# Kernel optimization log

Hardware: AMD Instinct MI355X
Metric: run time of the kernel (lower is better)

The kernel has to match this reference:

```python
import jax, jax.numpy as jnp
import numpy as np

EPS = 1e-6

def setup_inputs() -> dict:
    key = jax.random.key(0)
    ks = jax.random.split(key, 8)
    S, B, I, D, L = 1024, 16, 1024, 1024, 2
    std = np.sqrt(2.0 / (5.0 * I))
    inp = {
        "input": jax.random.normal(ks[0], (S, B, I), jnp.float32),
        "h0": jnp.zeros((L, B, D), jnp.float32),
        "extra0": jnp.zeros((L, B, 3 * D), jnp.float32),
        "W0": jax.random.normal(ks[1], (4 * D, I), jnp.float32) * std,
        "b0": jnp.zeros((4 * D,), jnp.float32).at[2 * D:3 * D].set(
            jax.random.uniform(ks[2], (D,), jnp.float32, 3.0, 6.0)),
        "r0": jnp.zeros((4 * D,), jnp.float32),
        "W1": jax.random.normal(ks[3], (4 * D, D), jnp.float32) * std,
        "b1": jnp.zeros((4 * D,), jnp.float32).at[2 * D:3 * D].set(
            jax.random.uniform(ks[4], (D,), jnp.float32, 3.0, 6.0)),
        "r1": jnp.zeros((4 * D,), jnp.float32),
    }
    return inp

def _cell(x, c, n, h, m, W, b, r):
    # x: (B, in), states: (B, D), W: (4D, in), b/r: (4D,)
    D = h.shape[-1]
    pre = x @ W.T + b  # (B, 4D)
    rz, ri, rf, ro = jnp.split(r, 4)
    z_pre = pre[:, 0 * D:1 * D] + rz * h
    i_pre = pre[:, 1 * D:2 * D] + ri * h
    f_pre = pre[:, 2 * D:3 * D] + rf * h
    o_pre = pre[:, 3 * D:4 * D] + ro * h
    z_t = jnp.tanh(z_pre)
    o_t = jax.nn.sigmoid(o_pre)
    m_new = jnp.maximum(f_pre + m, i_pre)
    f_t = jnp.exp(f_pre + m - m_new)
    i_t = jnp.exp(i_pre - m_new)
    c_new = f_t * c + i_t * z_t
    n_new = f_t * n + i_t
    h_new = o_t * (c_new / (jnp.abs(n_new) + EPS))
    return h_new, c_new, n_new, m_new

def _run(input, h0, extra0, params):
    D = h0.shape[-1]
    c0 = extra0[:, :, 0 * D:1 * D]
    n0 = extra0[:, :, 1 * D:2 * D]
    m0 = extra0[:, :, 2 * D:3 * D]

    def step(carry, x_t):
        h, c, n, m = carry  # each (L, B, D)
        x = x_t
        hs, cs, ns, ms = [], [], [], []
        for l, (W, b, r) in enumerate(params):
            h_new, c_new, n_new, m_new = _cell(x, c[l], n[l], h[l], m[l], W, b, r)
            hs.append(h_new); cs.append(c_new); ns.append(n_new); ms.append(m_new)
            x = h_new
        carry = (jnp.stack(hs), jnp.stack(cs), jnp.stack(ns), jnp.stack(ms))
        return carry, x

    (h_f, c_f, n_f, m_f), output = jax.lax.scan(step, (h0, c0, n0, m0), input)
    extra_f = jnp.concatenate([c_f, n_f, m_f], axis=-1)
    return output, h_f, extra_f

def reference(input, h0, extra0, W0, b0, r0, W1, b1, r1):
    params = [(W0, b0, r0), (W1, b1, r1)]
    return _run(input, h0, extra0, params)
```

## Files before the change

### kernel.cpp

```cpp
#include <hip/hip_runtime.h>
#include <hip/hip_bf16.h>

#define S_LEN  1024
#define BATCH  16
#define IDIM   1024
#define DDIM   1024
#define NG     4096
#define BD     16384
#define LAYERS 2
#define PF     16
#define PFP    8
#define NSEG   8

typedef __attribute__((ext_vector_type(8))) short   short8;
typedef __attribute__((ext_vector_type(4))) float   floatx4;
typedef __attribute__((address_space(1))) void      as1_void;
typedef __attribute__((address_space(3))) void      as3_void;

#define L2E  1.4426950408889634f
#define LN2  0.6931471805599453f

#define EXP2F(x) exp2f(x)

static __device__ __forceinline__ unsigned short f2bf(float x) {
    unsigned int u = __float_as_uint(x);
    return (unsigned short)((u + 0x7fffu + ((u >> 16) & 1u)) >> 16);
}

__global__ void detect_dtype(const void* w, int* flag)
{
    const __hip_bfloat16* p = (const __hip_bfloat16*)w;
    float mx = 0.0f;
    for (int i = threadIdx.x; i < 4096; i += 64) {
        float v = __bfloat162float(p[i]);
        float a = fabsf(v);
        if (!(a == a)) a = 1e30f;
        mx = fmaxf(mx, a);
    }
#pragma unroll
    for (int o = 32; o > 0; o >>= 1)
        mx = fmaxf(mx, __shfl_down(mx, o, 64));
    if (threadIdx.x == 0) *flag = (mx > 1e3f) ? 1 : 0;
}

__global__ void to_bf16(const void* src, size_t elem_off, const int* flag,
                        unsigned short* dst, int n)
{
    const int i = blockIdx.x * 256 + threadIdx.x;
    if (i >= n) return;
    if (*flag) dst[i] = f2bf(((const float*)src)[elem_off + i]);
    else       dst[i] = ((const unsigned short*)src)[elem_off + i];
}

__global__ void prep_small(const void* __restrict__ h0,
                           const void* __restrict__ extra0,
                           const void* __restrict__ b0s, const void* __restrict__ r0s,
                           const void* __restrict__ b1s, const void* __restrict__ r1s,
                           const int* __restrict__ flag,
                           float* __restrict__ state,
                           float* __restrict__ pb,
                           int* __restrict__ rflag)
{
    const int blk = blockIdx.x;
    const int fl = *flag;

    if (blk < 128) {
        const int idx = blk * 256 + threadIdx.x;
        const int l  = idx / BD;
        const int bd = idx % BD;
        const int b = bd >> 10, d = bd & 1023;
        float* st = state + (size_t)l * 4 * BD;
        const size_t eoff = ((size_t)l * BATCH + b) * (3 * DDIM);
        float cv, nv, mv, hv;
        if (fl) {
            const float* e = (const float*)extra0 + eoff;
            cv = e[d]; nv = e[DDIM + d]; mv = e[2 * DDIM + d];
            hv = ((const float*)h0)[(size_t)l * BD + bd];
        } else {
            const __hip_bfloat16* e = (const __hip_bfloat16*)extra0 + eoff;
            cv = __bfloat162float(e[d]);
            nv = __bfloat162float(e[DDIM + d]);
            mv = __bfloat162float(e[2 * DDIM + d]);
            hv = __bfloat162float(((const __hip_bfloat16*)h0)[(size_t)l * BD + bd]);
        }
        st[0 * BD + bd] = cv;
        st[1 * BD + bd] = nv;
        st[2 * BD + bd] = mv * L2E;
        st[3 * BD + bd] = hv;
        return;
    }

    const int which = blk - 128;
    const void* src = (which == 0) ? b0s : (which == 1) ? r0s
                    : (which == 2) ? b1s : r1s;
    float* dst = pb + (size_t)which * NG;
    int nz = 0;
#pragma unroll
    for (int j = 0; j < NG / 256; j++) {
        const int i = j * 256 + threadIdx.x;
        float v;
        if (fl) {
            v = ((const float*)src)[i];
            nz |= (v != 0.0f);
        } else {
            const unsigned short u = ((const unsigned short*)src)[i];
            nz |= ((u & 0x7fffu) != 0);
            v = __bfloat162float(((const __hip_bfloat16*)src)[i]);
        }
        dst[i] = v;
    }
    if (which == 1 || which == 3) {
        __shared__ int s[4];
        const int w = threadIdx.x >> 6;
        const int any = __any(nz) ? 1 : 0;
        if ((threadIdx.x & 63) == 0) s[w] = any;
        __syncthreads();
        if (threadIdx.x == 0) rflag[which >> 1] = !(s[0] | s[1] | s[2] | s[3]);
    }
}

__global__ __launch_bounds__(256, 2)
void gemm_bias(const __hip_bfloat16* __restrict__ A,
               const __hip_bfloat16* __restrict__ W,
               const float* __restrict__ bias,
               unsigned short* __restrict__ out,
               const int* __restrict__ rflag)
{
    constexpr int K = 1024;
    __shared__ alignas(16) __hip_bfloat16 sA[128 * 32];
    __shared__ alignas(16) __hip_bfloat16 sB[128 * 32];

    const int t  = threadIdx.x;
    const int m0 = blockIdx.y * 128;
    const int nb = blockIdx.x;
    const int lr = t & 15;
    const int q  = (t >> 4) & 3;
    const int w  = t >> 6;
    const int wm = w >> 1, wn = w & 1;
    const int sr = t >> 2;
    const int sk = (t & 3) * 8;

    floatx4 acc[4][4] = {};

    const __hip_bfloat16* Ab = A + (size_t)(m0 + sr) * K + sk;
    const int wrow = ((sr >> 5) << 10) + nb * 32 + (sr & 31);
    const __hip_bfloat16* Wb = W + (size_t)wrow * K + sk;

    for (int k0 = 0; k0 < K; k0 += 32) {
        __syncthreads();
        __builtin_amdgcn_global_load_lds((as1_void*)(Ab + k0),            (as3_void*)&sA[sr * 32 + sk],        16, 0, 0);
        __builtin_amdgcn_global_load_lds((as1_void*)(Ab + 64 * K + k0),   (as3_void*)&sA[(sr + 64) * 32 + sk], 16, 0, 0);
        __builtin_amdgcn_global_load_lds((as1_void*)(Wb + k0),            (as3_void*)&sB[sr * 32 + sk],        16, 0, 0);
        __builtin_amdgcn_global_load_lds((as1_void*)(Wb + 2048 * K + k0), (as3_void*)&sB[(sr + 64) * 32 + sk], 16, 0, 0);
        __syncthreads();

        short8 af[4], bf[4];
#pragma unroll
        for (int i = 0; i < 4; i++)
            af[i] = *(const short8*)&sA[(wm * 64 + i * 16 + lr) * 32 + q * 8];
#pragma unroll
        for (int j = 0; j < 4; j++)
            bf[j] = *(const short8*)&sB[(j * 32 + wn * 16 + lr) * 32 + q * 8];
#pragma unroll
        for (int i = 0; i < 4; i++)
#pragma unroll
            for (int j = 0; j < 4; j++)
                acc[i][j] = __builtin_amdgcn_mfma_f32_16x16x32_bf16(af[i], bf[j], acc[i][j], 0, 0, 0);
    }

    const int d = nb * 32 + wn * 16 + lr;
    const float sc[4] = {2.0f * L2E, L2E, L2E, L2E};
    float bb[4];
#pragma unroll
    for (int g = 0; g < 4; g++) bb[g] = sc[g] * bias[g * 1024 + d];

    const int rfast = *rflag;

#pragma unroll
    for (int i = 0; i < 4; i++) {
#pragma unroll
        for (int reg = 0; reg < 4; reg++) {
            const int row = m0 + wm * 64 + i * 16 + q * 4 + reg;
            float v[4];
#pragma unroll
            for (int g = 0; g < 4; g++)
                v[g] = acc[i][g][reg] * sc[g] + bb[g];
            if (rfast) {
                const float zv = v[0];
                const float e2 = EXP2F(-fabsf(zv));
                v[0] = copysignf((1.0f - e2) * __builtin_amdgcn_rcpf(1.0f + e2), zv);
                v[3] = __builtin_amdgcn_rcpf(1.0f + EXP2F(-v[3]));
            }
            union { unsigned short us[4]; uint2 u2; } pk;
#pragma unroll
            for (int g = 0; g < 4; g++) pk.us[g] = f2bf(v[g]);
            *(uint2*)(out + (size_t)row * NG + d * 4) = pk.u2;
        }
    }
}

__global__ void scan_passA(const unsigned int* __restrict__ pre,
                           const int* __restrict__ rflag,
                           float* __restrict__ smry, int T)
{
    if (!*rflag) return;
    const int gid = blockIdx.x * 256 + threadIdx.x;
    const int chain = gid & (BD - 1);
    const int seg = gid >> 14;
    const int SEG = T >> 3;
    const int b = chain >> 10, d = chain & 1023;

    const size_t stp = 32768;
    const unsigned int* p = pre + (size_t)b * 2048 + (size_t)d * 2
                              + (size_t)(seg * SEG) * stp;

    float alpha = 0.0f, mu = -3e38f, Bh = 0.0f, Nh = 0.0f;

    unsigned int k0[PFP], k1[PFP];
#pragma unroll
    for (int u = 0; u < PFP; u++) {
        const uint2 v = *(const uint2*)(p + (size_t)u * stp);
        k0[u] = v.x; k1[u] = v.y;
    }

    for (int t = 0; t < SEG; t += PFP) {
#pragma unroll
        for (int u = 0; u < PFP; u++) {
            const float zt = __uint_as_float(k0[u] << 16);
            const float i2 = __uint_as_float(k0[u] & 0xffff0000u);
            const float f2 = __uint_as_float(k1[u] << 16);

            const uint2 nv = *(const uint2*)(p + (size_t)(t + u + PFP) * stp);
            k0[u] = nv.x; k1[u] = nv.y;

            alpha += f2;
            const float e  = i2 - alpha;
            const float mn = fmaxf(mu, e);
            const float s  = EXP2F(mu - mn);
            const float w  = EXP2F(e - mn);
            Bh = fmaf(Bh, s, w * zt);
            Nh = fmaf(Nh, s, w);
            mu = mn;
        }
    }

    smry[0 * NSEG * BD + seg * BD + chain] = alpha;
    smry[1 * NSEG * BD + seg * BD + chain] = alpha + mu;
    smry[2 * NSEG * BD + seg * BD + chain] = Bh;
    smry[3 * NSEG * BD + seg * BD + chain] = Nh;
}

__global__ void scan_mid(const float* __restrict__ smry,
                         const int* __restrict__ rflag,
                         const float* __restrict__ state,
                         float* __restrict__ seginit, int T)
{
    if (!*rflag) return;
    const int idx = blockIdx.x * 256 + threadIdx.x;
    float c  = state[0 * BD + idx];
    float n  = state[1 * BD + idx];
    float m2 = state[2 * BD + idx];
#pragma unroll
    for (int s = 0; s < NSEG; s++) {
        seginit[0 * NSEG * BD + s * BD + idx] = c;
        seginit[1 * NSEG * BD + s * BD + idx] = n;
        seginit[2 * NSEG * BD + s * BD + idx] = m2;
        const float A    = smry[0 * NSEG * BD + s * BD + idx];
        const float bmax = smry[1 * NSEG * BD + s * BD + idx];
        const float Bh   = smry[2 * NSEG * BD + s * BD + idx];
        const float Nh   = smry[3 * NSEG * BD + s * BD + idx];
        const float mn = fmaxf(m2 + A, bmax);
        const float sc = EXP2F(m2 + A - mn);
        const float w  = EXP2F(bmax - mn);
        c  = fmaf(sc, c, w * Bh);
        n  = fmaf(sc, n, w * Nh);
        m2 = mn;
    }
}

template<int MODE>
__global__ void scan_passB(const unsigned int* __restrict__ pre,
                           const float* __restrict__ seginit,
                           const int* __restrict__ rflag,
                           float* __restrict__ state,
                           unsigned short* __restrict__ hseq,
                           void* __restrict__ gout, size_t gout_eoff,
                           const int* __restrict__ flag, int T)
{
    if (!*rflag) return;
    const int gid = blockIdx.x * 256 + threadIdx.x;
    const int chain = gid & (BD - 1);
    const int seg = gid >> 14;
    const int SEG = T >> 3;
    const int t0s = seg * SEG;
    const int b = chain >> 10, d = chain & 1023;
    const int fl = *flag;

    float c  = seginit[0 * NSEG * BD + seg * BD + chain];
    float n  = seginit[1 * NSEG * BD + seg * BD + chain];
    float m2 = seginit[2 * NSEG * BD + seg * BD + chain];

    const size_t stp = 32768;
    const unsigned int* p = pre + (size_t)b * 2048 + (size_t)d * 2
                              + (size_t)t0s * stp;

    unsigned short* hb = hseq + (size_t)b * DDIM + d + (size_t)t0s * BD;
    float*          fo = (float*)gout + gout_eoff + (size_t)b * DDIM + d + (size_t)t0s * BD;
    unsigned short* bo = (unsigned short*)gout + gout_eoff + (size_t)b * DDIM + d + (size_t)t0s * BD;

    float h = 0.0f;
    unsigned int k0[PFP], k1[PFP];
#pragma unroll
    for (int u = 0; u < PFP; u++) {
        const uint2 v = *(const uint2*)(p + (size_t)u * stp);
        k0[u] = v.x; k1[u] = v.y;
    }

    for (int t = 0; t < SEG; t += PFP) {
#pragma unroll
        for (int u = 0; u < PFP; u++) {
            const float zt = __uint_as_float(k0[u] << 16);
            const float i2 = __uint_as_float(k0[u] & 0xffff0000u);
            const float f2 = __uint_as_float(k1[u] << 16);
            const float ot = __uint_as_float(k1[u] & 0xffff0000u);

            const uint2 nv = *(const uint2*)(p + (size_t)(t + u + PFP) * stp);
            k0[u] = nv.x; k1[u] = nv.y;

            const float fm = f2 + m2;
            const float mn = fmaxf(fm, i2);
            const float ft = EXP2F(fm - mn);
            const float it = EXP2F(i2 - mn);

            c  = fmaf(ft, c, it * zt);
            n  = fmaf(ft, n, it);
            m2 = mn;
            h  = ot * c * __builtin_amdgcn_rcpf(fabsf(n) + 1e-6f);

            const size_t toff = (size_t)(t + u) * BD;
            if (MODE == 0)      hb[toff] = f2bf(h);
            else if (fl)        fo[toff] = h;
            else                bo[toff] = f2bf(h);
        }
    }

    if (seg == NSEG - 1) {
        state[0 * BD + chain] = c;
        state[1 * BD + chain] = n;
        state[2 * BD + chain] = m2;
        state[3 * BD + chain] = h;
    }
}

template<int MODE>
__global__ void slstm_scan(const unsigned int* __restrict__ pre,
                           const float* __restrict__ r,
                           float* __restrict__ state,
                           unsigned short* __restrict__ hseq,
                           void* __restrict__ gout, size_t gout_eoff,
                           const int* __restrict__ flag,
                           const int* __restrict__ rflag, int T, int pgate)
{
    const int rfast = *rflag;
    if (pgate && rfast) return;

    const int idx = blockIdx.x * 64 + threadIdx.x;
    const int b = idx >> 10;
    const int d = idx & 1023;
    const int fl = *flag;

    const float rz = r[d]            * (2.0f * L2E);
    const float ri = r[DDIM + d]     * L2E;
    const float rf = r[2 * DDIM + d] * L2E;
    const float ro = r[3 * DDIM + d] * L2E;

    float c  = state[0 * BD + idx];
    float n  = state[1 * BD + idx];
    float m2 = state[2 * BD + idx];
    float h  = state[3 * BD + idx];

    const size_t stp = 32768;
    const unsigned int* p = pre + (size_t)b * 2048 + (size_t)d * 2;

    unsigned short* hb = hseq + (size_t)b * DDIM + d;
    float*          fo = (float*)gout + gout_eoff + (size_t)b * DDIM + d;
    unsigned short* bo = (unsigned short*)gout + gout_eoff + (size_t)b * DDIM + d;

    unsigned int k0[PF], k1[PF];
#pragma unroll
    for (int u = 0; u < PF; u++) {
        const uint2 v = *(const uint2*)(p + (size_t)u * stp);
        k0[u] = v.x; k1[u] = v.y;
    }

    if (rfast) {
        for (int t8 = 0; t8 < T; t8 += PF) {
#pragma unroll
            for (int u = 0; u < PF; u++) {
                const float zt = __uint_as_float(k0[u] << 16);
                const float i2 = __uint_as_float(k0[u] & 0xffff0000u);
                const float f2 = __uint_as_float(k1[u] << 16);
                const float ot = __uint_as_float(k1[u] & 0xffff0000u);

                const uint2 nv = *(const uint2*)(p + (size_t)(t8 + u + PF) * stp);
                k0[u] = nv.x; k1[u] = nv.y;

                const float fm = f2 + m2;
                const float mn = fmaxf(fm, i2);
                const float ft = EXP2F(fm - mn);
                const float it = EXP2F(i2 - mn);

                c  = fmaf(ft, c, it * zt);
                n  = fmaf(ft, n, it);
                m2 = mn;
                h  = ot * c * __builtin_amdgcn_rcpf(fabsf(n) + 1e-6f);

                const size_t toff = (size_t)(t8 + u) * BD;
                if (MODE == 0)      hb[toff] = f2bf(h);
                else if (fl)        fo[toff] = h;
                else                bo[toff] = f2bf(h);
            }
        }
    } else {
        for (int t8 = 0; t8 < T; t8 += PF) {
#pragma unroll
            for (int u = 0; u < PF; u++) {
                float z2 = __uint_as_float(k0[u] << 16);
                float i2 = __uint_as_float(k0[u] & 0xffff0000u);
                float f2 = __uint_as_float(k1[u] << 16);
                float o2 = __uint_as_float(k1[u] & 0xffff0000u);

                const uint2 nv = *(const uint2*)(p + (size_t)(t8 + u + PF) * stp);
                k0[u] = nv.x; k1[u] = nv.y;

                z2 = fmaf(rz, h, z2);
                i2 = fmaf(ri, h, i2);
                f2 = fmaf(rf, h, f2);
                o2 = fmaf(ro, h, o2);

                const float fm = f2 + m2;
                const float mn = fmaxf(fm, i2);
                const float ft = EXP2F(fm - mn);
                const float it = EXP2F(i2 - mn);

                const float e2 = EXP2F(-fabsf(z2));
                const float zt = copysignf((1.0f - e2) * __builtin_amdgcn_rcpf(1.0f + e2), z2);
                const float ot = __builtin_amdgcn_rcpf(1.0f + EXP2F(-o2));

                c  = ft * c + it * zt;
                n  = ft * n + it;
                m2 = mn;
                h  = ot * c * __builtin_amdgcn_rcpf(fabsf(n) + 1e-6f);

                const size_t toff = (size_t)(t8 + u) * BD;
                if (MODE == 0)      hb[toff] = f2bf(h);
                else if (fl)        fo[toff] = h;
                else                bo[toff] = f2bf(h);
            }
        }
    }

    state[0 * BD + idx] = c;
    state[1 * BD + idx] = n;
    state[2 * BD + idx] = m2;
    state[3 * BD + idx] = h;
}

__global__ void finalize(const float* __restrict__ state,
                         void* __restrict__ out,
                         const int* __restrict__ flag)
{
    const int idx = blockIdx.x * 256 + threadIdx.x;
    const int l  = idx / BD;
    const int bd = idx % BD;
    const int b = bd >> 10, d = bd & 1023;
    const float* st = state + (size_t)l * 4 * BD;
    const float cv = st[0 * BD + bd], nv = st[1 * BD + bd];
    const float mv = st[2 * BD + bd] * LN2;
    const float hv = st[3 * BD + bd];

    const size_t hoff = (size_t)S_LEN * BD + idx;
    const size_t eoff = (size_t)S_LEN * BD + (size_t)LAYERS * BD
                      + ((size_t)l * BATCH + b) * (3 * DDIM);
    if (*flag) {
        float* o = (float*)out;
        o[hoff] = hv;
        o[eoff + d] = cv; o[eoff + DDIM + d] = nv; o[eoff + 2 * DDIM + d] = mv;
    } else {
        unsigned short* o = (unsigned short*)out;
        o[hoff] = f2bf(hv);
        o[eoff + d]            = f2bf(cv);
        o[eoff + DDIM + d]     = f2bf(nv);
        o[eoff + 2 * DDIM + d] = f2bf(mv);
    }
}

__global__ void zero_out_k(void* __restrict__ out, const int* __restrict__ flag,
                           int out_size)
{
    const size_t i = (size_t)blockIdx.x * 256 + threadIdx.x;
    const size_t nb = (size_t)out_size * ((*flag) ? 4 : 2);
    char* o = (char*)out;
    for (size_t j = i * 4; j < (i + 1) * 4 && j < nb; j++) o[j] = 0;
}

extern "C" void kernel_launch(void* const* d_in, const int* in_sizes, int n_in,
                              void* d_out, int out_size, void* d_ws, size_t ws_size,
                              hipStream_t stream)
{
    const void* input  = d_in[0];
    const void* h0     = d_in[1];
    const void* extra0 = d_in[2];
    const void* W0     = d_in[3];
    const void* b0     = d_in[4];
    const void* r0     = d_in[5];
    const void* W1     = d_in[6];
    const void* b1     = d_in[7];
    const void* r1     = d_in[8];

    const size_t FLAG_B  = 256;
    const size_t STATE_B = (size_t)LAYERS * 4 * BD * 4;
    const size_t W_B     = (size_t)NG * IDIM * 2;
    const size_t PB_B    = (size_t)4 * NG * 4;
    const size_t SM_B    = (size_t)4 * NSEG * BD * 4;
    const size_t SI_B    = (size_t)3 * NSEG * BD * 4;
    const size_t FIXED   = FLAG_B + STATE_B + 2 * W_B + PB_B + SM_B + SI_B;

    int T = 0;
    for (int cand = S_LEN; cand >= 8; cand >>= 1) {
        size_t need = FIXED
                    + (size_t)cand * BD * 2
                    + (size_t)cand * BD * 2
                    + (size_t)(cand + PF) * BATCH * NG * 2;
        if (need <= ws_size) { T = cand; break; }
    }

    char* ws = (char*)d_ws;
    int*   flag  = (int*)ws;
    int*   rflag = flag + 1;
    float* state = (float*)(ws + FLAG_B);
    __hip_bfloat16* W0b = (__hip_bfloat16*)(ws + FLAG_B + STATE_B);
    __hip_bfloat16* W1b = W0b + (size_t)NG * IDIM;
    float* pb    = (float*)(ws + FLAG_B + STATE_B + 2 * W_B);
    float* b0f = pb, *r0f = pb + NG, *b1f = pb + 2 * NG, *r1f = pb + 3 * NG;
    float* smry    = (float*)(ws + FLAG_B + STATE_B + 2 * W_B + PB_B);
    float* seginit = smry + (size_t)4 * NSEG * BD;
    unsigned short* Ain  = (unsigned short*)(ws + FIXED);
    unsigned short* hseq = Ain + (size_t)T * BD;
    unsigned short* pre  = hseq + (size_t)T * BD;

    detect_dtype<<<dim3(1), dim3(64), 0, stream>>>(W0, flag);

    if (T == 0) {
        zero_out_k<<<dim3((out_size + 255) / 256), dim3(256), 0, stream>>>(d_out, flag, out_size);
        return;
    }

    const int WN = NG * IDIM;
    to_bf16<<<dim3(WN / 256), dim3(256), 0, stream>>>(W0, 0, flag, (unsigned short*)W0b, WN);
    to_bf16<<<dim3(WN / 256), dim3(256), 0, stream>>>(W1, 0, flag, (unsigned short*)W1b, WN);

    prep_small<<<dim3(132), dim3(256), 0, stream>>>(h0, extra0, b0, r0, b1, r1,
                                                    flag, state, pb, rflag);

    const dim3 gemmGrid(32, (T * BATCH) / 128);
    const dim3 scanGrid(BD / 64);
    const dim3 passGrid((BD * NSEG) / 256);
    const dim3 midGrid(BD / 256);
    const int  nch = S_LEN / T;
    const int  useP = (T >= 64) ? 1 : 0;

    for (int ch = 0; ch < nch; ch++) {
        const int t0 = ch * T;

        to_bf16<<<dim3((T * BD) / 256), dim3(256), 0, stream>>>(
            input, (size_t)t0 * BD, flag, Ain, T * BD);

        gemm_bias<<<gemmGrid, 256, 0, stream>>>((const __hip_bfloat16*)Ain, W0b, b0f, pre, rflag + 0);
        if (useP) {
            scan_passA<<<passGrid, 256, 0, stream>>>((const unsigned int*)pre, rflag + 0, smry, T);
            scan_mid<<<midGrid, 256, 0, stream>>>(smry, rflag + 0, state, seginit, T);
            scan_passB<0><<<passGrid, 256, 0, stream>>>((const unsigned int*)pre, seginit, rflag + 0,
                                                        state, hseq, (void*)0, 0, flag, T);
        }
        slstm_scan<0><<<scanGrid, 64, 0, stream>>>((const unsigned int*)pre, r0f, state,
                                                   hseq, (void*)0, 0, flag, rflag + 0, T, useP);

        gemm_bias<<<gemmGrid, 256, 0, stream>>>((const __hip_bfloat16*)hseq, W1b, b1f, pre, rflag + 1);
        if (useP) {
            scan_passA<<<passGrid, 256, 0, stream>>>((const unsigned int*)pre, rflag + 1, smry, T);
            scan_mid<<<midGrid, 256, 0, stream>>>(smry, rflag + 1, state + 4 * BD, seginit, T);
            scan_passB<1><<<passGrid, 256, 0, stream>>>((const unsigned int*)pre, seginit, rflag + 1,
                                                        state + 4 * BD, (unsigned short*)0,
                                                        d_out, (size_t)t0 * BD, flag, T);
        }
        slstm_scan<1><<<scanGrid, 64, 0, stream>>>((const unsigned int*)pre, r1f,
                                                   state + 4 * BD, (unsigned short*)0,
                                                   d_out, (size_t)t0 * BD, flag, rflag + 1, T, useP);
    }

    finalize<<<dim3(LAYERS * BD / 256), dim3(256), 0, stream>>>(state, d_out, flag);
}
```

Measured before the change: 637.6 us.

## Double-buffer GEMM LDS tiles and process two chains per thread in scan passes

The GEMM now stages the next K-slice into a second LDS buffer while computing on the current one, using a vmcnt wait and raw barriers in place of two __syncthreads per iteration. This is meant to hide global-load latency. Separately, scan_passA and scan_passB each handle two adjacent chains per thread with 16-byte loads and paired stores, halving the grid. That gives more independent work per thread and wider memory accesses, but exposes fewer threads for latency hiding and doubles LDS use in the GEMM, which may lower occupancy.

```diff
diff --git a/kernel.cpp b/kernel.cpp
--- a/kernel.cpp
+++ b/kernel.cpp
@@ -127,8 +127,8 @@
                const int* __restrict__ rflag)
 {
     constexpr int K = 1024;
-    __shared__ alignas(16) __hip_bfloat16 sA[128 * 32];
-    __shared__ alignas(16) __hip_bfloat16 sB[128 * 32];
+    __shared__ alignas(16) __hip_bfloat16 sA[2][128 * 32];
+    __shared__ alignas(16) __hip_bfloat16 sB[2][128 * 32];
 
     const int t  = threadIdx.x;
     const int m0 = blockIdx.y * 128;
@@ -146,27 +146,41 @@
     const int wrow = ((sr >> 5) << 10) + nb * 32 + (sr & 31);
     const __hip_bfloat16* Wb = W + (size_t)wrow * K + sk;
 
+#define STAGE(bi, kk) do {                                                                                        \
+    __builtin_amdgcn_global_load_lds((as1_void*)(Ab + (kk)),            (as3_void*)&sA[bi][sr * 32 + sk],        16, 0, 0); \
+    __builtin_amdgcn_global_load_lds((as1_void*)(Ab + 64 * K + (kk)),   (as3_void*)&sA[bi][(sr + 64) * 32 + sk], 16, 0, 0); \
+    __builtin_amdgcn_global_load_lds((as1_void*)(Wb + (kk)),            (as3_void*)&sB[bi][sr * 32 + sk],        16, 0, 0); \
+    __builtin_amdgcn_global_load_lds((as1_void*)(Wb + 2048 * K + (kk)), (as3_void*)&sB[bi][(sr + 64) * 32 + sk], 16, 0, 0); \
+} while (0)
+
+    STAGE(0, 0);
+    int cur = 0;
     for (int k0 = 0; k0 < K; k0 += 32) {
-        __syncthreads();
-        __builtin_amdgcn_global_load_lds((as1_void*)(Ab + k0),            (as3_void*)&sA[sr * 32 + sk],        16, 0, 0);
-        __builtin_amdgcn_global_load_lds((as1_void*)(Ab + 64 * K + k0),   (as3_void*)&sA[(sr + 64) * 32 + sk], 16, 0, 0);
-        __builtin_amdgcn_global_load_lds((as1_void*)(Wb + k0),            (as3_void*)&sB[sr * 32 + sk],        16, 0, 0);
-        __builtin_amdgcn_global_load_lds((as1_void*)(Wb + 2048 * K + k0), (as3_void*)&sB[(sr + 64) * 32 + sk], 16, 0, 0);
-        __syncthreads();
-
+        const int kn = (k0 + 32) & (K - 1);
+        if (cur == 0) STAGE(1, kn); else STAGE(0, kn);
+
+        asm volatile("s_waitcnt vmcnt(4)" ::: "memory");
+        __builtin_amdgcn_s_barrier();
+
+        const __hip_bfloat16* cA = sA[cur];
+        const __hip_bfloat16* cB = sB[cur];
         short8 af[4], bf[4];
 #pragma unroll
         for (int i = 0; i < 4; i++)
-            af[i] = *(const short8*)&sA[(wm * 64 + i * 16 + lr) * 32 + q * 8];
+            af[i] = *(const short8*)&cA[(wm * 64 + i * 16 + lr) * 32 + q * 8];
 #pragma unroll
         for (int j = 0; j < 4; j++)
-            bf[j] = *(const short8*)&sB[(j * 32 + wn * 16 + lr) * 32 + q * 8];
+            bf[j] = *(const short8*)&cB[(j * 32 + wn * 16 + lr) * 32 + q * 8];
 #pragma unroll
         for (int i = 0; i < 4; i++)
 #pragma unroll
             for (int j = 0; j < 4; j++)
                 acc[i][j] = __builtin_amdgcn_mfma_f32_16x16x32_bf16(af[i], bf[j], acc[i][j], 0, 0, 0);
-    }
+
+        __builtin_amdgcn_s_barrier();
+        cur ^= 1;
+    }
+#undef STAGE
 
     const int d = nb * 32 + wn * 16 + lr;
     const float sc[4] = {2.0f * L2E, L2E, L2E, L2E};
@@ -205,49 +219,61 @@
 {
     if (!*rflag) return;
     const int gid = blockIdx.x * 256 + threadIdx.x;
-    const int chain = gid & (BD - 1);
-    const int seg = gid >> 14;
+    const int pr  = gid & (BD / 2 - 1);
+    const int seg = gid >> 13;
     const int SEG = T >> 3;
+    const int chain = pr * 2;
     const int b = chain >> 10, d = chain & 1023;
 
     const size_t stp = 32768;
     const unsigned int* p = pre + (size_t)b * 2048 + (size_t)d * 2
                               + (size_t)(seg * SEG) * stp;
 
-    float alpha = 0.0f, mu = -3e38f, Bh = 0.0f, Nh = 0.0f;
-
-    unsigned int k0[PFP], k1[PFP];
-#pragma unroll
-    for (int u = 0; u < PFP; u++) {
-        const uint2 v = *(const uint2*)(p + (size_t)u * stp);
-        k0[u] = v.x; k1[u] = v.y;
-    }
+    float al0 = 0.0f, mu0 = -3e38f, B0 = 0.0f, N0 = 0.0f;
+    float al1 = 0.0f, mu1 = -3e38f, B1 = 0.0f, N1 = 0.0f;
+
+    uint4 k[PFP];
+#pragma unroll
+    for (int u = 0; u < PFP; u++) k[u] = *(const uint4*)(p + (size_t)u * stp);
 
     for (int t = 0; t < SEG; t += PFP) {
 #pragma unroll
         for (int u = 0; u < PFP; u++) {
-            const float zt = __uint_as_float(k0[u] << 16);
-            const float i2 = __uint_as_float(k0[u] & 0xffff0000u);
-            const float f2 = __uint_as_float(k1[u] << 16);
-
-            const uint2 nv = *(const uint2*)(p + (size_t)(t + u + PFP) * stp);
-            k0[u] = nv.x; k1[u] = nv.y;
-
-            alpha += f2;
-            const float e  = i2 - alpha;
-            const float mn = fmaxf(mu, e);
-            const float s  = EXP2F(mu - mn);
-            const float w  = EXP2F(e - mn);
-            Bh = fmaf(Bh, s, w * zt);
-            Nh = fmaf(Nh, s, w);
-            mu = mn;
-        }
-    }
-
-    smry[0 * NSEG * BD + seg * BD + chain] = alpha;
-    smry[1 * NSEG * BD + seg * BD + chain] = alpha + mu;
-    smry[2 * NSEG * BD + seg * BD + chain] = Bh;
-    smry[3 * NSEG * BD + seg * BD + chain] = Nh;
+            const uint4 kv = k[u];
+            k[u] = *(const uint4*)(p + (size_t)(t + u + PFP) * stp);
+            {
+                const float zt = __uint_as_float(kv.x << 16);
+                const float i2 = __uint_as_float(kv.x & 0xffff0000u);
+                const float f2 = __uint_as_float(kv.y << 16);
+                al0 += f2;
+                const float e  = i2 - al0;
+                const float mn = fmaxf(mu0, e);
+                const float s  = EXP2F(mu0 - mn);
+                const float ww = EXP2F(e - mn);
+                B0 = fmaf(B0, s, ww * zt);
+                N0 = fmaf(N0, s, ww);
+                mu0 = mn;
+            }
+            {
+                const float zt = __uint_as_float(kv.z << 16);
+                const float i2 = __uint_as_float(kv.z & 0xffff0000u);
+                const float f2 = __uint_as_float(kv.w << 16);
+                al1 += f2;
+                const float e  = i2 - al1;
+                const float mn = fmaxf(mu1, e);
+                const float s  = EXP2F(mu1 - mn);
+                const float ww = EXP2F(e - mn);
+                B1 = fmaf(B1, s, ww * zt);
+                N1 = fmaf(N1, s, ww);
+                mu1 = mn;
+            }
+        }
+    }
+
+    *(float2*)&smry[0 * NSEG * BD + seg * BD + chain] = make_float2(al0, al1);
+    *(float2*)&smry[1 * NSEG * BD + seg * BD + chain] = make_float2(al0 + mu0, al1 + mu1);
+    *(float2*)&smry[2 * NSEG * BD + seg * BD + chain] = make_float2(B0, B1);
+    *(float2*)&smry[3 * NSEG * BD + seg * BD + chain] = make_float2(N0, N1);
 }
 
 __global__ void scan_mid(const float* __restrict__ smry,
@@ -289,66 +315,82 @@
 {
     if (!*rflag) return;
     const int gid = blockIdx.x * 256 + threadIdx.x;
-    const int chain = gid & (BD - 1);
-    const int seg = gid >> 14;
+    const int pr  = gid & (BD / 2 - 1);
+    const int seg = gid >> 13;
     const int SEG = T >> 3;
     const int t0s = seg * SEG;
+    const int chain = pr * 2;
     const int b = chain >> 10, d = chain & 1023;
     const int fl = *flag;
 
-    float c  = seginit[0 * NSEG * BD + seg * BD + chain];
-    float n  = seginit[1 * NSEG * BD + seg * BD + chain];
-    float m2 = seginit[2 * NSEG * BD + seg * BD + chain];
+    float2 cc = *(const float2*)&seginit[0 * NSEG * BD + seg * BD + chain];
+    float2 nn = *(const float2*)&seginit[1 * NSEG * BD + seg * BD + chain];
+    float2 mm = *(const float2*)&seginit[2 * NSEG * BD + seg * BD + chain];
+    float c0 = cc.x, c1 = cc.y, n0 = nn.x, n1 = nn.y, m0 = mm.x, m1 = mm.y;
 
     const size_t stp = 32768;
     const unsigned int* p = pre + (size_t)b * 2048 + (size_t)d * 2
                               + (size_t)t0s * stp;
 
-    unsigned short* hb = hseq + (size_t)b * DDIM + d + (size_t)t0s * BD;
-    float*          fo = (float*)gout + gout_eoff + (size_t)b * DDIM + d + (size_t)t0s * BD;
-    unsigned short* bo = (unsigned short*)gout + gout_eoff + (size_t)b * DDIM + d + (size_t)t0s * BD;
-
-    float h = 0.0f;
-    unsigned int k0[PFP], k1[PFP];
-#pragma unroll
-    for (int u = 0; u < PFP; u++) {
-        const uint2 v = *(const uint2*)(p + (size_t)u * stp);
-        k0[u] = v.x; k1[u] = v.y;
-    }
+    unsigned int*   hb = (unsigned int*)(hseq + (size_t)b * DDIM + d) ;
+    float*          fo = (float*)gout + gout_eoff + (size_t)b * DDIM + d;
+    unsigned int*   bo = (unsigned int*)((unsigned short*)gout + gout_eoff + (size_t)b * DDIM + d);
+
+    float h0 = 0.0f, h1 = 0.0f;
+    uint4 k[PFP];
+#pragma unroll
+    for (int u = 0; u < PFP; u++) k[u] = *(const uint4*)(p + (size_t)u * stp);
 
     for (int t = 0; t < SEG; t += PFP) {
 #pragma unroll
         for (int u = 0; u < PFP; u++) {
-            const float zt = __uint_as_float(k0[u] << 16);
-            const float i2 = __uint_as_float(k0[u] & 0xffff0000u);
-            const float f2 = __uint_as_float(k1[u] << 16);
-            const float ot = __uint_as_float(k1[u] & 0xffff0000u);
-
-            const uint2 nv = *(const uint2*)(p + (size_t)(t + u + PFP) * stp);
-            k0[u] = nv.x; k1[u] = nv.y;
-
-            const float fm = f2 + m2;
-            const float mn = fmaxf(fm, i2);
-            const float ft = EXP2F(fm - mn);
-            const float it = EXP2F(i2 - mn);
-
-            c  = fmaf(ft, c, it * zt);
-            n  = fmaf(ft, n, it);
-            m2 = mn;
-            h  = ot * c * __builtin_amdgcn_rcpf(fabsf(n) + 1e-6f);
-
-            const size_t toff = (size_t)(t + u) * BD;
-            if (MODE == 0)      hb[toff] = f2bf(h);
-            else if (fl)        fo[toff] = h;
-            else                bo[toff] = f2bf(h);
+            const uint4 kv = k[u];
+            k[u] = *(const uint4*)(p + (size_t)(t + u + PFP) * stp);
+            {
+                const float zt = __uint_as_float(kv.x << 16);
+                const float i2 = __uint_as_float(kv.x & 0xffff0000u);
+                const float f2 = __uint_as_float(kv.y << 16);
+                const float ot = __uint_as_float(kv.y & 0xffff0000u);
+                const float fm = f2 + m0;
+                const float mn = fmaxf(fm, i2);
+                const float ft = EXP2F(fm - mn);
+                const float it = EXP2F(i2 - mn);
+                c0 = fmaf(ft, c0, it * zt);
+                n0 = fmaf(ft, n0, it);
+                m0 = mn;
+                h0 = ot * c0 * __builtin_amdgcn_rcpf(fabsf(n0) + 1e-6f);
+            }
+            {
+                const float zt = __uint_as_float(kv.z << 16);
+                const float i2 = __uint_as_float(kv.z & 0xffff0000u);
+                const float f2 = __uint_as_float(kv.w << 16);
+                const float ot = __uint_as_float(kv.w & 0xffff0000u);
+                const float fm = f2 + m1;
+                const float mn = fmaxf(fm, i2);
+                const float ft = EXP2F(fm - mn);
+                const float it = EXP2F(i2 - mn);
+                c1 = fmaf(ft, c1, it * zt);
+                n1 = fmaf(ft, n1, it);
+                m1 = mn;
+                h1 = ot * c1 * __builtin_amdgcn_rcpf(fabsf(n1) + 1e-6f);
+            }
+
+            const size_t toff = (size_t)(t0s + t + u) * BD;
+            if (MODE == 0) {
+                hb[(toff >> 1)] = (unsigned int)f2bf(h0) | ((unsigned int)f2bf(h1) << 16);
+            } else if (fl) {
+                *(float2*)(fo + toff) = make_float2(h0, h1);
+            } else {
+                bo[(toff >> 1)] = (unsigned int)f2bf(h0) | ((unsigned int)f2bf(h1) << 16);
+            }
         }
     }
 
     if (seg == NSEG - 1) {
-        state[0 * BD + chain] = c;
-        state[1 * BD + chain] = n;
-        state[2 * BD + chain] = m2;
-        state[3 * BD + chain] = h;
+        *(float2*)&state[0 * BD + chain] = make_float2(c0, c1);
+        *(float2*)&state[1 * BD + chain] = make_float2(n0, n1);
+        *(float2*)&state[2 * BD + chain] = make_float2(m0, m1);
+        *(float2*)&state[3 * BD + chain] = make_float2(h0, h1);
     }
 }
 
@@ -565,7 +607,7 @@
 
     const dim3 gemmGrid(32, (T * BATCH) / 128);
     const dim3 scanGrid(BD / 64);
-    const dim3 passGrid((BD * NSEG) / 256);
+    const dim3 passGrid((BD * NSEG / 2) / 256);
     const dim3 midGrid(BD / 256);
     const int  nch = S_LEN / T;
     const int  useP = (T >= 64) ? 1 : 0;
```

Result: no change. 643.6 us (+0.9%).

## Store gate pre-activations chain-major and use more scan segments

Applied to the files above, without the earlier changes.

The GEMM epilogue now writes gate pre-activations in a chain-major layout, padded per chain (tpad = T+PF), instead of time-major. Each scan thread can then read consecutive timesteps with 16-byte vector loads rather than strided 8-byte loads. The segment count for the parallel scan goes from 8 to 32 to expose more threads per chain, and seginit storage is folded into the summary buffer. The trade-off is scattered 8-byte stores in the GEMM epilogue and a stricter condition for taking the parallel path.

```diff
diff --git a/kernel.cpp b/kernel.cpp
--- a/kernel.cpp
+++ b/kernel.cpp
@@ -10,7 +10,7 @@
 #define LAYERS 2
 #define PF     16
 #define PFP    8
-#define NSEG   8
+#define NSEG   32
 
 typedef __attribute__((ext_vector_type(8))) short   short8;
 typedef __attribute__((ext_vector_type(4))) float   floatx4;
@@ -124,7 +124,7 @@
                const __hip_bfloat16* __restrict__ W,
                const float* __restrict__ bias,
                unsigned short* __restrict__ out,
-               const int* __restrict__ rflag)
+               const int* __restrict__ rflag, int tpad)
 {
     constexpr int K = 1024;
     __shared__ alignas(16) __hip_bfloat16 sA[128 * 32];
@@ -181,6 +181,8 @@
 #pragma unroll
         for (int reg = 0; reg < 4; reg++) {
             const int row = m0 + wm * 64 + i * 16 + q * 4 + reg;
+            const int trow = row >> 4;
+            const int b    = row & 15;
             float v[4];
 #pragma unroll
             for (int g = 0; g < 4; g++)
@@ -194,66 +196,65 @@
             union { unsigned short us[4]; uint2 u2; } pk;
 #pragma unroll
             for (int g = 0; g < 4; g++) pk.us[g] = f2bf(v[g]);
-            *(uint2*)(out + (size_t)row * NG + d * 4) = pk.u2;
+            const size_t chain = (size_t)((b << 10) + d);
+            *(uint2*)(out + (chain * tpad + trow) * 4) = pk.u2;
         }
     }
 }
 
 __global__ void scan_passA(const unsigned int* __restrict__ pre,
                            const int* __restrict__ rflag,
-                           float* __restrict__ smry, int T)
+                           float* __restrict__ smry, int T, int tpad)
 {
     if (!*rflag) return;
     const int gid = blockIdx.x * 256 + threadIdx.x;
     const int chain = gid & (BD - 1);
     const int seg = gid >> 14;
-    const int SEG = T >> 3;
-    const int b = chain >> 10, d = chain & 1023;
-
-    const size_t stp = 32768;
-    const unsigned int* p = pre + (size_t)b * 2048 + (size_t)d * 2
-                              + (size_t)(seg * SEG) * stp;
-
-    float alpha = 0.0f, mu = -3e38f, Bh = 0.0f, Nh = 0.0f;
-
-    unsigned int k0[PFP], k1[PFP];
-#pragma unroll
-    for (int u = 0; u < PFP; u++) {
-        const uint2 v = *(const uint2*)(p + (size_t)u * stp);
-        k0[u] = v.x; k1[u] = v.y;
-    }
-
-    for (int t = 0; t < SEG; t += PFP) {
+    const int SEG = T / NSEG;
+    const int NU  = SEG >> 1;
+
+    const uint4* p4 = (const uint4*)((const unsigned long long*)pre
+                                     + (size_t)chain * tpad) + seg * NU;
+
+    float al = 0.0f, mu = -3e38f, Bh = 0.0f, Nh = 0.0f;
+
+    uint4 k[PFP];
+#pragma unroll
+    for (int u = 0; u < PFP; u++) k[u] = p4[u];
+
+    for (int j = 0; j < NU; j += PFP) {
 #pragma unroll
         for (int u = 0; u < PFP; u++) {
-            const float zt = __uint_as_float(k0[u] << 16);
-            const float i2 = __uint_as_float(k0[u] & 0xffff0000u);
-            const float f2 = __uint_as_float(k1[u] << 16);
-
-            const uint2 nv = *(const uint2*)(p + (size_t)(t + u + PFP) * stp);
-            k0[u] = nv.x; k1[u] = nv.y;
-
-            alpha += f2;
-            const float e  = i2 - alpha;
-            const float mn = fmaxf(mu, e);
-            const float s  = EXP2F(mu - mn);
-            const float w  = EXP2F(e - mn);
-            Bh = fmaf(Bh, s, w * zt);
-            Nh = fmaf(Nh, s, w);
-            mu = mn;
-        }
-    }
-
-    smry[0 * NSEG * BD + seg * BD + chain] = alpha;
-    smry[1 * NSEG * BD + seg * BD + chain] = alpha + mu;
+            const uint4 kv = k[u];
+            k[u] = p4[j + u + PFP];
+#pragma unroll
+            for (int hlf = 0; hlf < 2; hlf++) {
+                const unsigned int a = hlf ? kv.z : kv.x;
+                const unsigned int bwd = hlf ? kv.w : kv.y;
+                const float zt = __uint_as_float(a << 16);
+                const float i2 = __uint_as_float(a & 0xffff0000u);
+                const float f2 = __uint_as_float(bwd << 16);
+                al += f2;
+                const float e  = i2 - al;
+                const float mn = fmaxf(mu, e);
+                const float s  = EXP2F(mu - mn);
+                const float ww = EXP2F(e - mn);
+                Bh = fmaf(Bh, s, ww * zt);
+                Nh = fmaf(Nh, s, ww);
+                mu = mn;
+            }
+        }
+    }
+
+    smry[0 * NSEG * BD + seg * BD + chain] = al;
+    smry[1 * NSEG * BD + seg * BD + chain] = al + mu;
     smry[2 * NSEG * BD + seg * BD + chain] = Bh;
     smry[3 * NSEG * BD + seg * BD + chain] = Nh;
 }
 
-__global__ void scan_mid(const float* __restrict__ smry,
+__global__ void scan_mid(float* __restrict__ smry,
                          const int* __restrict__ rflag,
-                         const float* __restrict__ state,
-                         float* __restrict__ seginit, int T)
+                         const float* __restrict__ state, int T)
 {
     if (!*rflag) return;
     const int idx = blockIdx.x * 256 + threadIdx.x;
@@ -262,13 +263,13 @@
     float m2 = state[2 * BD + idx];
 #pragma unroll
     for (int s = 0; s < NSEG; s++) {
-        seginit[0 * NSEG * BD + s * BD + idx] = c;
-        seginit[1 * NSEG * BD + s * BD + idx] = n;
-        seginit[2 * NSEG * BD + s * BD + idx] = m2;
         const float A    = smry[0 * NSEG * BD + s * BD + idx];
         const float bmax = smry[1 * NSEG * BD + s * BD + idx];
         const float Bh   = smry[2 * NSEG * BD + s * BD + idx];
         const float Nh   = smry[3 * NSEG * BD + s * BD + idx];
+        smry[0 * NSEG * BD + s * BD + idx] = c;
+        smry[1 * NSEG * BD + s * BD + idx] = n;
+        smry[2 * NSEG * BD + s * BD + idx] = m2;
         const float mn = fmaxf(m2 + A, bmax);
         const float sc = EXP2F(m2 + A - mn);
         const float w  = EXP2F(bmax - mn);
@@ -280,67 +281,67 @@
 
 template<int MODE>
 __global__ void scan_passB(const unsigned int* __restrict__ pre,
-                           const float* __restrict__ seginit,
+                           const float* __restrict__ smry,
                            const int* __restrict__ rflag,
                            float* __restrict__ state,
                            unsigned short* __restrict__ hseq,
                            void* __restrict__ gout, size_t gout_eoff,
-                           const int* __restrict__ flag, int T)
+                           const int* __restrict__ flag, int T, int tpad)
 {
     if (!*rflag) return;
     const int gid = blockIdx.x * 256 + threadIdx.x;
     const int chain = gid & (BD - 1);
     const int seg = gid >> 14;
-    const int SEG = T >> 3;
+    const int SEG = T / NSEG;
+    const int NU  = SEG >> 1;
     const int t0s = seg * SEG;
-    const int b = chain >> 10, d = chain & 1023;
     const int fl = *flag;
 
-    float c  = seginit[0 * NSEG * BD + seg * BD + chain];
-    float n  = seginit[1 * NSEG * BD + seg * BD + chain];
-    float m2 = seginit[2 * NSEG * BD + seg * BD + chain];
-
-    const size_t stp = 32768;
-    const unsigned int* p = pre + (size_t)b * 2048 + (size_t)d * 2
-                              + (size_t)t0s * stp;
-
-    unsigned short* hb = hseq + (size_t)b * DDIM + d + (size_t)t0s * BD;
-    float*          fo = (float*)gout + gout_eoff + (size_t)b * DDIM + d + (size_t)t0s * BD;
-    unsigned short* bo = (unsigned short*)gout + gout_eoff + (size_t)b * DDIM + d + (size_t)t0s * BD;
+    float c  = smry[0 * NSEG * BD + seg * BD + chain];
+    float n  = smry[1 * NSEG * BD + seg * BD + chain];
+    float m2 = smry[2 * NSEG * BD + seg * BD + chain];
+
+    const uint4* p4 = (const uint4*)((const unsigned long long*)pre
+                                     + (size_t)chain * tpad) + seg * NU;
+
+    unsigned short* hb = hseq + chain;
+    float*          fo = (float*)gout + gout_eoff + chain;
+    unsigned short* bo = (unsigned short*)gout + gout_eoff + chain;
 
     float h = 0.0f;
-    unsigned int k0[PFP], k1[PFP];
-#pragma unroll
-    for (int u = 0; u < PFP; u++) {
-        const uint2 v = *(const uint2*)(p + (size_t)u * stp);
-        k0[u] = v.x; k1[u] = v.y;
-    }
-
-    for (int t = 0; t < SEG; t += PFP) {
+    uint4 k[PFP];
+#pragma unroll
+    for (int u = 0; u < PFP; u++) k[u] = p4[u];
+
+    for (int j = 0; j < NU; j += PFP) {
 #pragma unroll
         for (int u = 0; u < PFP; u++) {
-            const float zt = __uint_as_float(k0[u] << 16);
-            const float i2 = __uint_as_float(k0[u] & 0xffff0000u);
-            const float f2 = __uint_as_float(k1[u] << 16);
-            const float ot = __uint_as_float(k1[u] & 0xffff0000u);
-
-            const uint2 nv = *(const uint2*)(p + (size_t)(t + u + PFP) * stp);
-            k0[u] = nv.x; k1[u] = nv.y;
-
-            const float fm = f2 + m2;
-            const float mn = fmaxf(fm, i2);
-            const float ft = EXP2F(fm - mn);
-            const float it = EXP2F(i2 - mn);
-
-            c  = fmaf(ft, c, it * zt);
-            n  = fmaf(ft, n, it);
-            m2 = mn;
-            h  = ot * c * __builtin_amdgcn_rcpf(fabsf(n) + 1e-6f);
-
-            const size_t toff = (size_t)(t + u) * BD;
-            if (MODE == 0)      hb[toff] = f2bf(h);
-            else if (fl)        fo[toff] = h;
-            else                bo[toff] = f2bf(h);
+            const uint4 kv = k[u];
+            k[u] = p4[j + u + PFP];
+#pragma unroll
+            for (int hlf = 0; hlf < 2; hlf++) {
+                const unsigned int a = hlf ? kv.z : kv.x;
+                const unsigned int bwd = hlf ? kv.w : kv.y;
+                const float zt = __uint_as_float(a << 16);
+                const float i2 = __uint_as_float(a & 0xffff0000u);
+                const float f2 = __uint_as_float(bwd << 16);
+                const float ot = __uint_as_float(bwd & 0xffff0000u);
+
+                const float fm = f2 + m2;
+                const float mn = fmaxf(fm, i2);
+                const float ft = EXP2F(fm - mn);
+                const float it = EXP2F(i2 - mn);
+
+                c  = fmaf(ft, c, it * zt);
+                n  = fmaf(ft, n, it);
+                m2 = mn;
+                h  = ot * c * __builtin_amdgcn_rcpf(fabsf(n) + 1e-6f);
+
+                const size_t toff = (size_t)(t0s + 2 * (j + u) + hlf) * BD;
+                if (MODE == 0)      hb[toff] = f2bf(h);
+                else if (fl)        fo[toff] = h;
+                else                bo[toff] = f2bf(h);
+            }
         }
     }
 
@@ -359,13 +360,13 @@
                            unsigned short* __restrict__ hseq,
                            void* __restrict__ gout, size_t gout_eoff,
                            const int* __restrict__ flag,
-                           const int* __restrict__ rflag, int T, int pgate)
+                           const int* __restrict__ rflag, int T, int tpad,
+                           int pgate)
 {
     const int rfast = *rflag;
     if (pgate && rfast) return;
 
     const int idx = blockIdx.x * 64 + threadIdx.x;
-    const int b = idx >> 10;
     const int d = idx & 1023;
     const int fl = *flag;
 
@@ -379,17 +380,17 @@
     float m2 = state[2 * BD + idx];
     float h  = state[3 * BD + idx];
 
-    const size_t stp = 32768;
-    const unsigned int* p = pre + (size_t)b * 2048 + (size_t)d * 2;
-
-    unsigned short* hb = hseq + (size_t)b * DDIM + d;
-    float*          fo = (float*)gout + gout_eoff + (size_t)b * DDIM + d;
-    unsigned short* bo = (unsigned short*)gout + gout_eoff + (size_t)b * DDIM + d;
+    const uint2* p = (const uint2*)((const unsigned long long*)pre
+                                    + (size_t)idx * tpad);
+
+    unsigned short* hb = hseq + idx;
+    float*          fo = (float*)gout + gout_eoff + idx;
+    unsigned short* bo = (unsigned short*)gout + gout_eoff + idx;
 
     unsigned int k0[PF], k1[PF];
 #pragma unroll
     for (int u = 0; u < PF; u++) {
-        const uint2 v = *(const uint2*)(p + (size_t)u * stp);
+        const uint2 v = p[u];
         k0[u] = v.x; k1[u] = v.y;
     }
 
@@ -402,7 +403,7 @@
                 const float f2 = __uint_as_float(k1[u] << 16);
                 const float ot = __uint_as_float(k1[u] & 0xffff0000u);
 
-                const uint2 nv = *(const uint2*)(p + (size_t)(t8 + u + PF) * stp);
+                const uint2 nv = p[t8 + u + PF];
                 k0[u] = nv.x; k1[u] = nv.y;
 
                 const float fm = f2 + m2;
@@ -430,7 +431,7 @@
                 float f2 = __uint_as_float(k1[u] << 16);
                 float o2 = __uint_as_float(k1[u] & 0xffff0000u);
 
-                const uint2 nv = *(const uint2*)(p + (size_t)(t8 + u + PF) * stp);
+                const uint2 nv = p[t8 + u + PF];
                 k0[u] = nv.x; k1[u] = nv.y;
 
                 z2 = fmaf(rz, h, z2);
@@ -523,15 +524,14 @@
     const size_t W_B     = (size_t)NG * IDIM * 2;
     const size_t PB_B    = (size_t)4 * NG * 4;
     const size_t SM_B    = (size_t)4 * NSEG * BD * 4;
-    const size_t SI_B    = (size_t)3 * NSEG * BD * 4;
-    const size_t FIXED   = FLAG_B + STATE_B + 2 * W_B + PB_B + SM_B + SI_B;
+    const size_t FIXED   = FLAG_B + STATE_B + 2 * W_B + PB_B + SM_B;
 
     int T = 0;
     for (int cand = S_LEN; cand >= 8; cand >>= 1) {
         size_t need = FIXED
                     + (size_t)cand * BD * 2
                     + (size_t)cand * BD * 2
-                    + (size_t)(cand + PF) * BATCH * NG * 2;
+                    + (size_t)(cand + PF) * BD * 8;
         if (need <= ws_size) { T = cand; break; }
     }
 
@@ -543,8 +543,7 @@
     __hip_bfloat16* W1b = W0b + (size_t)NG * IDIM;
     float* pb    = (float*)(ws + FLAG_B + STATE_B + 2 * W_B);
     float* b0f = pb, *r0f = pb + NG, *b1f = pb + 2 * NG, *r1f = pb + 3 * NG;
-    float* smry    = (float*)(ws + FLAG_B + STATE_B + 2 * W_B + PB_B);
-    float* seginit = smry + (size_t)4 * NSEG * BD;
+    float* smry  = (float*)(ws + FLAG_B + STATE_B + 2 * W_B + PB_B);
     unsigned short* Ain  = (unsigned short*)(ws + FIXED);
     unsigned short* hseq = Ain + (size_t)T * BD;
     unsigned short* pre  = hseq + (size_t)T * BD;
@@ -563,12 +562,13 @@
     prep_small<<<dim3(132), dim3(256), 0, stream>>>(h0, extra0, b0, r0, b1, r1,
                                                     flag, state, pb, rflag);
 
+    const int  tpad = T + PF;
     const dim3 gemmGrid(32, (T * BATCH) / 128);
     const dim3 scanGrid(BD / 64);
     const dim3 passGrid((BD * NSEG) / 256);
     const dim3 midGrid(BD / 256);
     const int  nch = S_LEN / T;
-    const int  useP = (T >= 64) ? 1 : 0;
+    const int  useP = (T >= 512 && (T % (NSEG * 16)) == 0) ? 1 : 0;
 
     for (int ch = 0; ch < nch; ch++) {
         const int t0 = ch * T;
@@ -576,27 +576,27 @@
         to_bf16<<<dim3((T * BD) / 256), dim3(256), 0, stream>>>(
             input, (size_t)t0 * BD, flag, Ain, T * BD);
 
-        gemm_bias<<<gemmGrid, 256, 0, stream>>>((const __hip_bfloat16*)Ain, W0b, b0f, pre, rflag + 0);
+        gemm_bias<<<gemmGrid, 256, 0, stream>>>((const __hip_bfloat16*)Ain, W0b, b0f, pre, rflag + 0, tpad);
         if (useP) {
-            scan_passA<<<passGrid, 256, 0, stream>>>((const unsigned int*)pre, rflag + 0, smry, T);
-            scan_mid<<<midGrid, 256, 0, stream>>>(smry, rflag + 0, state, seginit, T);
-            scan_passB<0><<<passGrid, 256, 0, stream>>>((const unsigned int*)pre, seginit, rflag + 0,
-                                                        state, hseq, (void*)0, 0, flag, T);
+            scan_passA<<<passGrid, 256, 0, stream>>>((const unsigned int*)pre, rflag + 0, smry, T, tpad);
+            scan_mid<<<midGrid, 256, 0, stream>>>(smry, rflag + 0, state, T);
+            scan_passB<0><<<passGrid, 256, 0, stream>>>((const unsigned int*)pre, smry, rflag + 0,
+                                                        state, hseq, (void*)0, 0, flag, T, tpad);
         }
         slstm_scan<0><<<scanGrid, 64, 0, stream>>>((const unsigned int*)pre, r0f, state,
-                                                   hseq, (void*)0, 0, flag, rflag + 0, T, useP);
-
-        gemm_bias<<<gemmGrid, 256, 0, stream>>>((const __hip_bfloat16*)hseq, W1b, b1f, pre, rflag + 1);
+                                                   hseq, (void*)0, 0, flag, rflag + 0, T, tpad, useP);
+
+        gemm_bias<<<gemmGrid, 256, 0, stream>>>((const __hip_bfloat16*)hseq, W1b, b1f, pre, rflag + 1, tpad);
         if (useP) {
-            scan_passA<<<passGrid, 256, 0, stream>>>((const unsigned int*)pre, rflag + 1, smry, T);
-            scan_mid<<<midGrid, 256, 0, stream>>>(smry, rflag + 1, state + 4 * BD, seginit, T);
-            scan_passB<1><<<passGrid, 256, 0, stream>>>((const unsigned int*)pre, seginit, rflag + 1,
+            scan_passA<<<passGrid, 256, 0, stream>>>((const unsigned int*)pre, rflag + 1, smry, T, tpad);
+            scan_mid<<<midGrid, 256, 0, stream>>>(smry, rflag + 1, state + 4 * BD, T);
+            scan_passB<1><<<passGrid, 256, 0, stream>>>((const unsigned int*)pre, smry, rflag + 1,
                                                         state + 4 * BD, (unsigned short*)0,
-                                                        d_out, (size_t)t0 * BD, flag, T);
+                                                        d_out, (size_t)t0 * BD, flag, T, tpad);
         }
         slstm_scan<1><<<scanGrid, 64, 0, stream>>>((const unsigned int*)pre, r1f,
                                                    state + 4 * BD, (unsigned short*)0,
-                                                   d_out, (size_t)t0 * BD, flag, rflag + 1, T, useP);
+                                                   d_out, (size_t)t0 * BD, flag, rflag + 1, T, tpad, useP);
     }
 
     finalize<<<dim3(LAYERS * BD / 256), dim3(256), 0, stream>>>(state, d_out, flag);
```

Result: slower. 750.7 us (+17.7%).
